# Performance work log

Measured on AMD Instinct MI355X. Metric: run time of the kernel, lower is better.

## Reference

```python
import jax, jax.numpy as jnp
import numpy as np

HEADS = 16
HEAD_DIM = 64
QUAD_C = 5.0   # 2quad: exp(x) ~ (x + c)^2
EPS = 1e-6


def setup_inputs() -> dict:
    key = jax.random.key(0)
    k1, k2, k3 = jax.random.split(key, 3)
    B, T, H = 2, 2048, 1024
    x = jax.random.normal(k1, (B, T, H), dtype=jnp.float32)
    # scaled init to keep pre-activation scores sane
    Wqkv = jax.random.normal(k2, (H, 3 * H), dtype=jnp.float32) * (H ** -0.5)
    Wo = jax.random.normal(k3, (H, H), dtype=jnp.float32) * (H ** -0.5)
    tau = jnp.full((HEADS,), 5.0, dtype=jnp.float32)
    return {"x": x, "Wqkv": Wqkv, "Wo": Wo, "tau": tau}


def reference(x, Wqkv, Wo, tau):
    B, T, C = x.shape
    h, d = HEADS, HEAD_DIM
    qkv = x @ Wqkv                                  # [B,T,3C]
    q, k, v = jnp.split(qkv, 3, axis=-1)
    q = q.reshape(B, T, h, d).transpose(0, 2, 1, 3)  # [B,h,T,d]
    k = k.reshape(B, T, h, d).transpose(0, 2, 1, 3)
    v = v.reshape(B, T, h, d).transpose(0, 2, 1, 3)
    # tau-scaled scores
    s = jnp.einsum("bhqd,bhkd->bhqk", q, k) / (jnp.sqrt(jnp.float32(d)) * tau[None, :, None, None])
    # 2quad attention: (s + c)^2 normalized over keys (non-softmax)
    e = jnp.square(s + QUAD_C)                       # [B,h,T,T], >=0
    w = e / (jnp.sum(e, axis=-1, keepdims=True) + EPS)
    out = jnp.einsum("bhqk,bhkd->bhqd", w, v)        # [B,h,T,d]
    out = out.transpose(0, 2, 1, 3).reshape(B, T, C)
    return out @ Wo
```

## Files before the change

### kernel.cpp

```cpp
#include <hip/hip_runtime.h>
#include <hip/hip_bf16.h>


typedef unsigned short ushort_t;
typedef __attribute__((ext_vector_type(8))) short short8;
typedef __attribute__((ext_vector_type(4))) float f32x4;
typedef __attribute__((ext_vector_type(16))) float f32x16;

#define B_      2
#define T_      2048
#define C_      1024
#define HEADS_  16
#define D_      64

union frag_u { unsigned u[4]; short8 s8; };

__device__ __forceinline__ ushort_t f2bf(float f) {
  __hip_bfloat16 h = __float2bfloat16(f);
  return *reinterpret_cast<ushort_t*>(&h);
}

__device__ __forceinline__ unsigned cvt_pk_bf16(float lo, float hi) {
  unsigned r;
  asm("v_cvt_pk_bf16_f32 %0, %1, %2" : "=v"(r) : "v"(lo), "v"(hi));
  return r;
}

__device__ __forceinline__ void permlane32_swap(unsigned &a, unsigned &b) {
  asm volatile("v_permlane32_swap_b32 %0, %1" : "+v"(a), "+v"(b));
}

__device__ __forceinline__ f32x16 zero16() {
  f32x16 z;
#pragma unroll
  for (int i = 0; i < 16; ++i) z[i] = 0.f;
  return z;
}

__global__ __launch_bounds__(256) void cast_x_kernel(const float* __restrict__ x,
                                                     ushort_t* __restrict__ xb) {
  int i = blockIdx.x * 256 + threadIdx.x;
  float4 f = ((const float4*)x)[i];
  ushort_t* o = xb + (size_t)i * 4;
  o[0] = f2bf(f.x); o[1] = f2bf(f.y); o[2] = f2bf(f.z); o[3] = f2bf(f.w);
}

__global__ __launch_bounds__(256) void transpose_cast_w(const float* __restrict__ in,
                                                        ushort_t* __restrict__ out,
                                                        int R, int Cc) {
  __shared__ float tile[64][65];
  int rb = blockIdx.y, cb = blockIdx.x;
  int c = threadIdx.x & 63;
  int r0 = threadIdx.x >> 6;
#pragma unroll
  for (int i = 0; i < 16; ++i) {
    int r = r0 + i * 4;
    tile[r][c] = in[(size_t)(rb * 64 + r) * Cc + cb * 64 + c];
  }
  __syncthreads();
#pragma unroll
  for (int i = 0; i < 16; ++i) {
    int r = r0 + i * 4;
    out[(size_t)(cb * 64 + r) * R + rb * 64 + c] = f2bf(tile[c][r]);
  }
}

__global__ __launch_bounds__(256) void transpose_v_kernel(const ushort_t* __restrict__ v,
                                                          ushort_t* __restrict__ vT) {
  __shared__ ushort_t tile[64][72];
  int bh = blockIdx.y, tb = blockIdx.x;
  int c = threadIdx.x & 63;
  int r0 = threadIdx.x >> 6;
#pragma unroll
  for (int i = 0; i < 16; ++i) {
    int r = r0 + i * 4;
    tile[r][c] = v[((size_t)bh * T_ + tb * 64 + r) * D_ + c];
  }
  __syncthreads();
#pragma unroll
  for (int i = 0; i < 16; ++i) {
    int r = r0 + i * 4;
    vT[((size_t)bh * D_ + r) * T_ + tb * 64 + c] = tile[c][r];
  }
}

__device__ __forceinline__ void gemm_tile(const ushort_t* __restrict__ A,
                                          const ushort_t* __restrict__ Bt,
                                          int K, int tm, int tn,
                                          ushort_t* lds, f32x4 acc[4][4]) {
  const int tid = threadIdx.x;
  const int lane = tid & 63, wave = tid >> 6;
  const int wm = wave >> 1, wn = wave & 1;
  const int lr = lane & 15, lk = lane >> 4;
  ushort_t* As = lds;
  ushort_t* Bs = lds + 128 * 72;
  const ushort_t* Ag = A + (size_t)tm * 128 * K;
  const ushort_t* Bg = Bt + (size_t)tn * 128 * K;

  for (int kt = 0; kt < K; kt += 64) {
#pragma unroll
    for (int i = 0; i < 4; ++i) {
      int cch = tid + i * 256; int row = cch >> 3, kc = cch & 7;
      *(short8*)&As[row * 72 + kc * 8] =
          *(const short8*)&Ag[(size_t)row * K + kt + kc * 8];
    }
#pragma unroll
    for (int i = 0; i < 4; ++i) {
      int cch = tid + i * 256; int row = cch >> 3, kc = cch & 7;
      *(short8*)&Bs[row * 72 + kc * 8] =
          *(const short8*)&Bg[(size_t)row * K + kt + kc * 8];
    }
    __syncthreads();
#pragma unroll
    for (int kk = 0; kk < 64; kk += 32) {
      short8 a[4], b[4];
#pragma unroll
      for (int m = 0; m < 4; ++m)
        a[m] = *(const short8*)&As[(wm * 64 + m * 16 + lr) * 72 + kk + lk * 8];
#pragma unroll
      for (int n = 0; n < 4; ++n)
        b[n] = *(const short8*)&Bs[(wn * 64 + n * 16 + lr) * 72 + kk + lk * 8];
#pragma unroll
      for (int m = 0; m < 4; ++m)
#pragma unroll
        for (int n = 0; n < 4; ++n)
          acc[m][n] = __builtin_amdgcn_mfma_f32_16x16x32_bf16(a[m], b[n], acc[m][n], 0, 0, 0);
    }
    __syncthreads();
  }
}

__global__ __launch_bounds__(256) void gemm_qkv(const ushort_t* __restrict__ xb,
                                                const ushort_t* __restrict__ wT,
                                                ushort_t* __restrict__ qg,
                                                ushort_t* __restrict__ kg,
                                                ushort_t* __restrict__ vg) {
  __shared__ __align__(16) ushort_t lds[2 * 128 * 72];
  f32x4 acc[4][4];
#pragma unroll
  for (int m = 0; m < 4; ++m)
#pragma unroll
    for (int n = 0; n < 4; ++n) acc[m][n] = (f32x4){0.f, 0.f, 0.f, 0.f};

  gemm_tile(xb, wT, C_, blockIdx.y, blockIdx.x, lds, acc);

  const int lane = threadIdx.x & 63, wave = threadIdx.x >> 6;
  const int wm = wave >> 1, wn = wave & 1;
  const int lr = lane & 15, lk = lane >> 4;
#pragma unroll
  for (int m = 0; m < 4; ++m)
#pragma unroll
    for (int n = 0; n < 4; ++n)
#pragma unroll
      for (int r = 0; r < 4; ++r) {
        int row = blockIdx.y * 128 + wm * 64 + m * 16 + lk * 4 + r;
        int col = blockIdx.x * 128 + wn * 64 + n * 16 + lr;
        int b = row >> 11, t = row & 2047;
        int part = col >> 10, idx = col & 1023;
        int h = idx >> 6, j = idx & 63;
        ushort_t* dst = (part == 0) ? qg : (part == 1) ? kg : vg;
        dst[(((size_t)(b * HEADS_ + h)) * T_ + t) * D_ + j] = f2bf(acc[m][n][r]);
      }
}

__global__ __launch_bounds__(256) void gemm_out(const ushort_t* __restrict__ ab,
                                                const ushort_t* __restrict__ woT,
                                                float* __restrict__ out) {
  __shared__ __align__(16) ushort_t lds[2 * 128 * 72];
  f32x4 acc[4][4];
#pragma unroll
  for (int m = 0; m < 4; ++m)
#pragma unroll
    for (int n = 0; n < 4; ++n) acc[m][n] = (f32x4){0.f, 0.f, 0.f, 0.f};

  gemm_tile(ab, woT, C_, blockIdx.y, blockIdx.x, lds, acc);

  const int lane = threadIdx.x & 63, wave = threadIdx.x >> 6;
  const int wm = wave >> 1, wn = wave & 1;
  const int lr = lane & 15, lk = lane >> 4;
#pragma unroll
  for (int m = 0; m < 4; ++m)
#pragma unroll
    for (int n = 0; n < 4; ++n)
#pragma unroll
      for (int r = 0; r < 4; ++r) {
        int row = blockIdx.y * 128 + wm * 64 + m * 16 + lk * 4 + r;
        int col = blockIdx.x * 128 + wn * 64 + n * 16 + lr;
        out[(size_t)row * C_ + col] = acc[m][n][r];
      }
}

__global__ __launch_bounds__(256, 2) void attn_kernel(const ushort_t* __restrict__ qg,
                                                      const ushort_t* __restrict__ kg,
                                                      const ushort_t* __restrict__ vTg,
                                                      const float* __restrict__ tau,
                                                      ushort_t* __restrict__ attn_out) {
  __shared__ __align__(16) ushort_t kvbuf[128 * 72 + 64 * 136];
  __shared__ float denom_lds[2][2][2][32];
  ushort_t* Ks  = kvbuf;
  ushort_t* Vts = kvbuf + 128 * 72;

  const int tid = threadIdx.x, lane = tid & 63;
  const int w = tid >> 6, wq = w >> 1, wk = w & 1;
  const int l31 = lane & 31, hi = lane >> 5, hi8 = hi * 8;
  const int qt = blockIdx.x, bh = blockIdx.y;
  const int b = bh >> 4, h = bh & 15;
  const float inv = 1.0f / (8.0f * tau[h]);

  const ushort_t* kb_ = kg  + (size_t)bh * T_ * D_;
  const ushort_t* vb_ = vTg + (size_t)bh * D_ * T_;
  const ushort_t* qp  = qg  + ((size_t)bh * T_ + qt * 128 + wq * 64) * D_;

  short8 qf[2][4];
#pragma unroll
  for (int qb = 0; qb < 2; ++qb)
#pragma unroll
    for (int dc = 0; dc < 4; ++dc)
      qf[qb][dc] = *(const short8*)&qp[(qb * 32 + l31) * D_ + dc * 16 + hi8];

  f32x16 acc[2][2];
  acc[0][0] = zero16(); acc[0][1] = zero16();
  acc[1][0] = zero16(); acc[1][1] = zero16();
  float denomp[2] = {0.f, 0.f};

  for (int rnd = 0; rnd < T_ / 128; ++rnd) {
    const int kv0 = rnd * 128;
#pragma unroll
    for (int i = 0; i < 4; ++i) {
      int cch = tid + i * 256;
      int row = cch >> 3, kc = cch & 7;
      *(short8*)&Ks[row * 72 + kc * 8] =
          *(const short8*)&kb_[(size_t)(kv0 + row) * D_ + kc * 8];
    }
#pragma unroll
    for (int i = 0; i < 4; ++i) {
      int cch = tid + i * 256;
      int row = cch >> 4, kc = cch & 15;
      *(short8*)&Vts[row * 136 + kc * 8] =
          *(const short8*)&vb_[(size_t)row * T_ + kv0 + kc * 8];
    }
    __syncthreads();

#pragma unroll
    for (int kb = 0; kb < 2; ++kb) {
      const int krow0 = wk * 64 + kb * 32;
      f32x16 s[2]; s[0] = zero16(); s[1] = zero16();
#pragma unroll
      for (int dc = 0; dc < 4; ++dc) {
        short8 kf = *(const short8*)&Ks[(krow0 + l31) * 72 + dc * 16 + hi8];
        s[0] = __builtin_amdgcn_mfma_f32_32x32x16_bf16(kf, qf[0][dc], s[0], 0, 0, 0);
        s[1] = __builtin_amdgcn_mfma_f32_32x32x16_bf16(kf, qf[1][dc], s[1], 0, 0, 0);
      }

      frag_u ef[2][2];
#pragma unroll
      for (int qb = 0; qb < 2; ++qb) {
        float ev[16];
        float dsum = 0.f;
#pragma unroll
        for (int r = 0; r < 16; ++r) {
          float t = fmaf(s[qb][r], inv, 5.0f);
          ev[r] = t * t;
          dsum += ev[r];
        }
        denomp[qb] += dsum;
        unsigned P[8];
#pragma unroll
        for (int p = 0; p < 8; ++p) P[p] = cvt_pk_bf16(ev[2 * p], ev[2 * p + 1]);
        unsigned a0 = P[0], b0 = P[2]; permlane32_swap(a0, b0);
        unsigned a1 = P[1], b1 = P[3]; permlane32_swap(a1, b1);
        ef[qb][0].u[0] = a0; ef[qb][0].u[1] = a1; ef[qb][0].u[2] = b0; ef[qb][0].u[3] = b1;
        unsigned a2 = P[4], b2 = P[6]; permlane32_swap(a2, b2);
        unsigned a3 = P[5], b3 = P[7]; permlane32_swap(a3, b3);
        ef[qb][1].u[0] = a2; ef[qb][1].u[1] = a3; ef[qb][1].u[2] = b2; ef[qb][1].u[3] = b3;
      }

#pragma unroll
      for (int c = 0; c < 2; ++c)
#pragma unroll
        for (int db = 0; db < 2; ++db) {
          short8 vf = *(const short8*)&Vts[(db * 32 + l31) * 136 + krow0 + c * 16 + hi8];
          acc[0][db] = __builtin_amdgcn_mfma_f32_32x32x16_bf16(ef[0][c].s8, vf, acc[0][db], 0, 0, 0);
          acc[1][db] = __builtin_amdgcn_mfma_f32_32x32x16_bf16(ef[1][c].s8, vf, acc[1][db], 0, 0, 0);
        }
    }
    __syncthreads();
  }

#pragma unroll
  for (int qb = 0; qb < 2; ++qb) {
    float v = denomp[qb];
    v += __shfl_xor(v, 32);
    if (lane < 32) denom_lds[wk][wq][qb][l31] = v;
  }
  float* out_lds = (float*)kvbuf;
  if (wk == 1) {
#pragma unroll
    for (int qb = 0; qb < 2; ++qb)
#pragma unroll
      for (int db = 0; db < 2; ++db)
#pragma unroll
        for (int r = 0; r < 16; ++r) {
          int qr = qb * 32 + (r & 3) + 8 * (r >> 2) + 4 * hi;
          out_lds[(wq * 64 + qr) * 64 + db * 32 + l31] = acc[qb][db][r];
        }
  }
  __syncthreads();
  if (wk == 0) {
#pragma unroll
    for (int qb = 0; qb < 2; ++qb)
#pragma unroll
      for (int r = 0; r < 16; ++r) {
        int cr = (r & 3) + 8 * (r >> 2) + 4 * hi;
        int qr = qb * 32 + cr;
        float dt = denom_lds[0][wq][qb][cr] + denom_lds[1][wq][qb][cr];
        float dinv = 1.0f / (dt + 1e-6f);
#pragma unroll
        for (int db = 0; db < 2; ++db) {
          float val = acc[qb][db][r] + out_lds[(wq * 64 + qr) * 64 + db * 32 + l31];
          int grow = b * T_ + qt * 128 + wq * 64 + qr;
          attn_out[(size_t)grow * C_ + h * 64 + db * 32 + l31] = f2bf(val * dinv);
        }
      }
  }
}

extern "C" void kernel_launch(void* const* d_in, const int* in_sizes, int n_in,
                              void* d_out, int out_size, void* d_ws, size_t ws_size,
                              hipStream_t stream) {
  const float* x    = (const float*)d_in[0];
  const float* Wqkv = (const float*)d_in[1];
  const float* Wo   = (const float*)d_in[2];
  const float* tau  = (const float*)d_in[3];
  float* out = (float*)d_out;

  char* ws = (char*)d_ws;
  ushort_t* xb    = (ushort_t*)(ws);
  ushort_t* wqkvT = (ushort_t*)(ws + 8388608);
  ushort_t* woT   = (ushort_t*)(ws + 14680064);
  ushort_t* qg    = (ushort_t*)(ws + 16777216);
  ushort_t* kg    = (ushort_t*)(ws + 25165824);
  ushort_t* ab    = (ushort_t*)(ws + 33554432);
  ushort_t* vg  = (ushort_t*)d_out;
  ushort_t* vTg = (ushort_t*)d_out + 4194304;

  cast_x_kernel<<<4096, 256, 0, stream>>>(x, xb);
  transpose_cast_w<<<dim3(48, 16), 256, 0, stream>>>(Wqkv, wqkvT, 1024, 3072);
  transpose_cast_w<<<dim3(16, 16), 256, 0, stream>>>(Wo, woT, 1024, 1024);
  gemm_qkv<<<dim3(24, 32), 256, 0, stream>>>(xb, wqkvT, qg, kg, vg);
  transpose_v_kernel<<<dim3(32, 32), 256, 0, stream>>>(vg, vTg);
  attn_kernel<<<dim3(16, 32), 256, 0, stream>>>(qg, kg, vTg, tau, ab);
  gemm_out<<<dim3(8, 32), 256, 0, stream>>>(ab, woT, out);
}
```

Measured before the change: 126.1 us.

## Split attention work across 4 key-slice waves and use direct global-to-LDS loads in GEMMs

The attention kernel now gives each block 64 queries instead of 128, and its four waves each take a 32-key slice of every 128-key tile. The launch grid doubles to 1024 blocks and the occupancy hint rises to 4 blocks per CU. Partial accumulators are combined through a two-stage LDS tree reduction, which adds extra barriers and reloads each K/V tile for half as many queries. Separately, the GEMM tile loader switches to global_load_lds with an unpadded 64-wide LDS layout, skipping the register round trip. That layout may cause LDS bank conflicts on the fragment reads.

```diff
diff --git a/kernel.cpp b/kernel.cpp
--- a/kernel.cpp
+++ b/kernel.cpp
@@ -35,6 +35,12 @@
 #pragma unroll
   for (int i = 0; i < 16; ++i) z[i] = 0.f;
   return z;
+}
+
+__device__ __forceinline__ void gload_lds16(const ushort_t* g, ushort_t* l) {
+  __builtin_amdgcn_global_load_lds(
+      (const __attribute__((address_space(1))) unsigned*)(const void*)g,
+      (__attribute__((address_space(3))) unsigned*)(void*)l, 16, 0, 0);
 }
 
 __global__ __launch_bounds__(256) void cast_x_kernel(const float* __restrict__ x,
@@ -93,22 +99,18 @@
   const int wm = wave >> 1, wn = wave & 1;
   const int lr = lane & 15, lk = lane >> 4;
   ushort_t* As = lds;
-  ushort_t* Bs = lds + 128 * 72;
+  ushort_t* Bs = lds + 128 * 64;
   const ushort_t* Ag = A + (size_t)tm * 128 * K;
   const ushort_t* Bg = Bt + (size_t)tn * 128 * K;
 
   for (int kt = 0; kt < K; kt += 64) {
 #pragma unroll
     for (int i = 0; i < 4; ++i) {
-      int cch = tid + i * 256; int row = cch >> 3, kc = cch & 7;
-      *(short8*)&As[row * 72 + kc * 8] =
-          *(const short8*)&Ag[(size_t)row * K + kt + kc * 8];
-    }
-#pragma unroll
-    for (int i = 0; i < 4; ++i) {
-      int cch = tid + i * 256; int row = cch >> 3, kc = cch & 7;
-      *(short8*)&Bs[row * 72 + kc * 8] =
-          *(const short8*)&Bg[(size_t)row * K + kt + kc * 8];
+      int chunk = wave * 4 + i;
+      int eidx = chunk * 512 + lane * 8;
+      int row = eidx >> 6, col = eidx & 63;
+      gload_lds16(Ag + (size_t)row * K + kt + col, As + eidx);
+      gload_lds16(Bg + (size_t)row * K + kt + col, Bs + eidx);
     }
     __syncthreads();
 #pragma unroll
@@ -116,10 +118,10 @@
       short8 a[4], b[4];
 #pragma unroll
       for (int m = 0; m < 4; ++m)
-        a[m] = *(const short8*)&As[(wm * 64 + m * 16 + lr) * 72 + kk + lk * 8];
+        a[m] = *(const short8*)&As[(wm * 64 + m * 16 + lr) * 64 + kk + lk * 8];
 #pragma unroll
       for (int n = 0; n < 4; ++n)
-        b[n] = *(const short8*)&Bs[(wn * 64 + n * 16 + lr) * 72 + kk + lk * 8];
+        b[n] = *(const short8*)&Bs[(wn * 64 + n * 16 + lr) * 64 + kk + lk * 8];
 #pragma unroll
       for (int m = 0; m < 4; ++m)
 #pragma unroll
@@ -135,7 +137,7 @@
                                                 ushort_t* __restrict__ qg,
                                                 ushort_t* __restrict__ kg,
                                                 ushort_t* __restrict__ vg) {
-  __shared__ __align__(16) ushort_t lds[2 * 128 * 72];
+  __shared__ __align__(16) ushort_t lds[2 * 128 * 64];
   f32x4 acc[4][4];
 #pragma unroll
   for (int m = 0; m < 4; ++m)
@@ -166,7 +168,7 @@
 __global__ __launch_bounds__(256) void gemm_out(const ushort_t* __restrict__ ab,
                                                 const ushort_t* __restrict__ woT,
                                                 float* __restrict__ out) {
-  __shared__ __align__(16) ushort_t lds[2 * 128 * 72];
+  __shared__ __align__(16) ushort_t lds[2 * 128 * 64];
   f32x4 acc[4][4];
 #pragma unroll
   for (int m = 0; m < 4; ++m)
@@ -190,18 +192,18 @@
       }
 }
 
-__global__ __launch_bounds__(256, 2) void attn_kernel(const ushort_t* __restrict__ qg,
+__global__ __launch_bounds__(256, 4) void attn_kernel(const ushort_t* __restrict__ qg,
                                                       const ushort_t* __restrict__ kg,
                                                       const ushort_t* __restrict__ vTg,
                                                       const float* __restrict__ tau,
                                                       ushort_t* __restrict__ attn_out) {
   __shared__ __align__(16) ushort_t kvbuf[128 * 72 + 64 * 136];
-  __shared__ float denom_lds[2][2][2][32];
+  __shared__ float denom_lds[4][2][32];
   ushort_t* Ks  = kvbuf;
   ushort_t* Vts = kvbuf + 128 * 72;
 
   const int tid = threadIdx.x, lane = tid & 63;
-  const int w = tid >> 6, wq = w >> 1, wk = w & 1;
+  const int w = tid >> 6;
   const int l31 = lane & 31, hi = lane >> 5, hi8 = hi * 8;
   const int qt = blockIdx.x, bh = blockIdx.y;
   const int b = bh >> 4, h = bh & 15;
@@ -209,7 +211,7 @@
 
   const ushort_t* kb_ = kg  + (size_t)bh * T_ * D_;
   const ushort_t* vb_ = vTg + (size_t)bh * D_ * T_;
-  const ushort_t* qp  = qg  + ((size_t)bh * T_ + qt * 128 + wq * 64) * D_;
+  const ushort_t* qp  = qg  + ((size_t)bh * T_ + qt * 64) * D_;
 
   short8 qf[2][4];
 #pragma unroll
@@ -222,6 +224,8 @@
   acc[0][0] = zero16(); acc[0][1] = zero16();
   acc[1][0] = zero16(); acc[1][1] = zero16();
   float denomp[2] = {0.f, 0.f};
+
+  const int krow0 = w * 32;
 
   for (int rnd = 0; rnd < T_ / 128; ++rnd) {
     const int kv0 = rnd * 128;
@@ -241,49 +245,45 @@
     }
     __syncthreads();
 
-#pragma unroll
-    for (int kb = 0; kb < 2; ++kb) {
-      const int krow0 = wk * 64 + kb * 32;
-      f32x16 s[2]; s[0] = zero16(); s[1] = zero16();
-#pragma unroll
-      for (int dc = 0; dc < 4; ++dc) {
-        short8 kf = *(const short8*)&Ks[(krow0 + l31) * 72 + dc * 16 + hi8];
-        s[0] = __builtin_amdgcn_mfma_f32_32x32x16_bf16(kf, qf[0][dc], s[0], 0, 0, 0);
-        s[1] = __builtin_amdgcn_mfma_f32_32x32x16_bf16(kf, qf[1][dc], s[1], 0, 0, 0);
-      }
-
-      frag_u ef[2][2];
-#pragma unroll
-      for (int qb = 0; qb < 2; ++qb) {
-        float ev[16];
-        float dsum = 0.f;
-#pragma unroll
-        for (int r = 0; r < 16; ++r) {
-          float t = fmaf(s[qb][r], inv, 5.0f);
-          ev[r] = t * t;
-          dsum += ev[r];
-        }
-        denomp[qb] += dsum;
-        unsigned P[8];
-#pragma unroll
-        for (int p = 0; p < 8; ++p) P[p] = cvt_pk_bf16(ev[2 * p], ev[2 * p + 1]);
-        unsigned a0 = P[0], b0 = P[2]; permlane32_swap(a0, b0);
-        unsigned a1 = P[1], b1 = P[3]; permlane32_swap(a1, b1);
-        ef[qb][0].u[0] = a0; ef[qb][0].u[1] = a1; ef[qb][0].u[2] = b0; ef[qb][0].u[3] = b1;
-        unsigned a2 = P[4], b2 = P[6]; permlane32_swap(a2, b2);
-        unsigned a3 = P[5], b3 = P[7]; permlane32_swap(a3, b3);
-        ef[qb][1].u[0] = a2; ef[qb][1].u[1] = a3; ef[qb][1].u[2] = b2; ef[qb][1].u[3] = b3;
-      }
-
-#pragma unroll
-      for (int c = 0; c < 2; ++c)
-#pragma unroll
-        for (int db = 0; db < 2; ++db) {
-          short8 vf = *(const short8*)&Vts[(db * 32 + l31) * 136 + krow0 + c * 16 + hi8];
-          acc[0][db] = __builtin_amdgcn_mfma_f32_32x32x16_bf16(ef[0][c].s8, vf, acc[0][db], 0, 0, 0);
-          acc[1][db] = __builtin_amdgcn_mfma_f32_32x32x16_bf16(ef[1][c].s8, vf, acc[1][db], 0, 0, 0);
-        }
-    }
+    f32x16 s[2]; s[0] = zero16(); s[1] = zero16();
+#pragma unroll
+    for (int dc = 0; dc < 4; ++dc) {
+      short8 kf = *(const short8*)&Ks[(krow0 + l31) * 72 + dc * 16 + hi8];
+      s[0] = __builtin_amdgcn_mfma_f32_32x32x16_bf16(kf, qf[0][dc], s[0], 0, 0, 0);
+      s[1] = __builtin_amdgcn_mfma_f32_32x32x16_bf16(kf, qf[1][dc], s[1], 0, 0, 0);
+    }
+
+    frag_u ef[2][2];
+#pragma unroll
+    for (int qb = 0; qb < 2; ++qb) {
+      float ev[16];
+      float dsum = 0.f;
+#pragma unroll
+      for (int r = 0; r < 16; ++r) {
+        float t = fmaf(s[qb][r], inv, 5.0f);
+        ev[r] = t * t;
+        dsum += ev[r];
+      }
+      denomp[qb] += dsum;
+      unsigned P[8];
+#pragma unroll
+      for (int p = 0; p < 8; ++p) P[p] = cvt_pk_bf16(ev[2 * p], ev[2 * p + 1]);
+      unsigned a0 = P[0], b0 = P[2]; permlane32_swap(a0, b0);
+      unsigned a1 = P[1], b1 = P[3]; permlane32_swap(a1, b1);
+      ef[qb][0].u[0] = a0; ef[qb][0].u[1] = a1; ef[qb][0].u[2] = b0; ef[qb][0].u[3] = b1;
+      unsigned a2 = P[4], b2 = P[6]; permlane32_swap(a2, b2);
+      unsigned a3 = P[5], b3 = P[7]; permlane32_swap(a3, b3);
+      ef[qb][1].u[0] = a2; ef[qb][1].u[1] = a3; ef[qb][1].u[2] = b2; ef[qb][1].u[3] = b3;
+    }
+
+#pragma unroll
+    for (int c = 0; c < 2; ++c)
+#pragma unroll
+      for (int db = 0; db < 2; ++db) {
+        short8 vf = *(const short8*)&Vts[(db * 32 + l31) * 136 + krow0 + c * 16 + hi8];
+        acc[0][db] = __builtin_amdgcn_mfma_f32_32x32x16_bf16(ef[0][c].s8, vf, acc[0][db], 0, 0, 0);
+        acc[1][db] = __builtin_amdgcn_mfma_f32_32x32x16_bf16(ef[1][c].s8, vf, acc[1][db], 0, 0, 0);
+      }
     __syncthreads();
   }
 
@@ -291,10 +291,10 @@
   for (int qb = 0; qb < 2; ++qb) {
     float v = denomp[qb];
     v += __shfl_xor(v, 32);
-    if (lane < 32) denom_lds[wk][wq][qb][l31] = v;
+    if (lane < 32) denom_lds[w][qb][l31] = v;
   }
   float* out_lds = (float*)kvbuf;
-  if (wk == 1) {
+  if (w >= 2) {
 #pragma unroll
     for (int qb = 0; qb < 2; ++qb)
 #pragma unroll
@@ -302,23 +302,48 @@
 #pragma unroll
         for (int r = 0; r < 16; ++r) {
           int qr = qb * 32 + (r & 3) + 8 * (r >> 2) + 4 * hi;
-          out_lds[(wq * 64 + qr) * 64 + db * 32 + l31] = acc[qb][db][r];
+          out_lds[(w - 2) * 4096 + qr * 64 + db * 32 + l31] = acc[qb][db][r];
         }
   }
   __syncthreads();
-  if (wk == 0) {
+  if (w < 2) {
+#pragma unroll
+    for (int qb = 0; qb < 2; ++qb)
+#pragma unroll
+      for (int db = 0; db < 2; ++db)
+#pragma unroll
+        for (int r = 0; r < 16; ++r) {
+          int qr = qb * 32 + (r & 3) + 8 * (r >> 2) + 4 * hi;
+          acc[qb][db][r] += out_lds[w * 4096 + qr * 64 + db * 32 + l31];
+        }
+  }
+  __syncthreads();
+  if (w == 1) {
+#pragma unroll
+    for (int qb = 0; qb < 2; ++qb)
+#pragma unroll
+      for (int db = 0; db < 2; ++db)
+#pragma unroll
+        for (int r = 0; r < 16; ++r) {
+          int qr = qb * 32 + (r & 3) + 8 * (r >> 2) + 4 * hi;
+          out_lds[qr * 64 + db * 32 + l31] = acc[qb][db][r];
+        }
+  }
+  __syncthreads();
+  if (w == 0) {
 #pragma unroll
     for (int qb = 0; qb < 2; ++qb)
 #pragma unroll
       for (int r = 0; r < 16; ++r) {
         int cr = (r & 3) + 8 * (r >> 2) + 4 * hi;
         int qr = qb * 32 + cr;
-        float dt = denom_lds[0][wq][qb][cr] + denom_lds[1][wq][qb][cr];
+        float dt = denom_lds[0][qb][cr] + denom_lds[1][qb][cr] +
+                   denom_lds[2][qb][cr] + denom_lds[3][qb][cr];
         float dinv = 1.0f / (dt + 1e-6f);
 #pragma unroll
         for (int db = 0; db < 2; ++db) {
-          float val = acc[qb][db][r] + out_lds[(wq * 64 + qr) * 64 + db * 32 + l31];
-          int grow = b * T_ + qt * 128 + wq * 64 + qr;
+          float val = acc[qb][db][r] + out_lds[qr * 64 + db * 32 + l31];
+          int grow = b * T_ + qt * 64 + qr;
           attn_out[(size_t)grow * C_ + h * 64 + db * 32 + l31] = f2bf(val * dinv);
         }
       }
@@ -349,6 +374,6 @@
   transpose_cast_w<<<dim3(16, 16), 256, 0, stream>>>(Wo, woT, 1024, 1024);
   gemm_qkv<<<dim3(24, 32), 256, 0, stream>>>(xb, wqkvT, qg, kg, vg);
   transpose_v_kernel<<<dim3(32, 32), 256, 0, stream>>>(vg, vTg);
-  attn_kernel<<<dim3(16, 32), 256, 0, stream>>>(qg, kg, vTg, tau, ab);
+  attn_kernel<<<dim3(32, 32), 256, 0, stream>>>(qg, kg, vTg, tau, ab);
   gemm_out<<<dim3(8, 32), 256, 0, stream>>>(ab, woT, out);
 }
```

Measured after the change: 284.8 us. 2.26x slower.

## Fuse V transpose into QKV GEMM epilogue and shrink attention blocks

Applied to the files above, without the earlier changes.

The QKV GEMM epilogue now writes V directly in transposed [bh, d, t] layout, so the separate transpose kernel and its extra round trip through memory go away. The attention kernel is restructured to 128-thread blocks, each handling 64 queries with 64-key tiles. That removes the split-K reduction across waves through LDS and doubles the grid size. The trade-offs are that transposed V stores are strided and uncoalesced, and each block reuses K/V less since it serves fewer queries per tile.

```diff
diff --git a/kernel.cpp b/kernel.cpp
--- a/kernel.cpp
+++ b/kernel.cpp
@@ -62,25 +62,6 @@
   for (int i = 0; i < 16; ++i) {
     int r = r0 + i * 4;
     out[(size_t)(cb * 64 + r) * R + rb * 64 + c] = f2bf(tile[c][r]);
-  }
-}
-
-__global__ __launch_bounds__(256) void transpose_v_kernel(const ushort_t* __restrict__ v,
-                                                          ushort_t* __restrict__ vT) {
-  __shared__ ushort_t tile[64][72];
-  int bh = blockIdx.y, tb = blockIdx.x;
-  int c = threadIdx.x & 63;
-  int r0 = threadIdx.x >> 6;
-#pragma unroll
-  for (int i = 0; i < 16; ++i) {
-    int r = r0 + i * 4;
-    tile[r][c] = v[((size_t)bh * T_ + tb * 64 + r) * D_ + c];
-  }
-  __syncthreads();
-#pragma unroll
-  for (int i = 0; i < 16; ++i) {
-    int r = r0 + i * 4;
-    vT[((size_t)bh * D_ + r) * T_ + tb * 64 + c] = tile[c][r];
   }
 }
 
@@ -134,7 +115,7 @@
                                                 const ushort_t* __restrict__ wT,
                                                 ushort_t* __restrict__ qg,
                                                 ushort_t* __restrict__ kg,
-                                                ushort_t* __restrict__ vg) {
+                                                ushort_t* __restrict__ vTg) {
   __shared__ __align__(16) ushort_t lds[2 * 128 * 72];
   f32x4 acc[4][4];
 #pragma unroll
@@ -158,8 +139,11 @@
         int b = row >> 11, t = row & 2047;
         int part = col >> 10, idx = col & 1023;
         int h = idx >> 6, j = idx & 63;
-        ushort_t* dst = (part == 0) ? qg : (part == 1) ? kg : vg;
-        dst[(((size_t)(b * HEADS_ + h)) * T_ + t) * D_ + j] = f2bf(acc[m][n][r]);
+        ushort_t val = f2bf(acc[m][n][r]);
+        size_t bh = (size_t)(b * HEADS_ + h);
+        if (part == 0)      qg[(bh * T_ + t) * D_ + j] = val;
+        else if (part == 1) kg[(bh * T_ + t) * D_ + j] = val;
+        else                vTg[(bh * D_ + j) * T_ + t] = val;
       }
 }
 
@@ -190,18 +174,17 @@
       }
 }
 
-__global__ __launch_bounds__(256, 2) void attn_kernel(const ushort_t* __restrict__ qg,
+__global__ __launch_bounds__(128, 2) void attn_kernel(const ushort_t* __restrict__ qg,
                                                       const ushort_t* __restrict__ kg,
                                                       const ushort_t* __restrict__ vTg,
                                                       const float* __restrict__ tau,
                                                       ushort_t* __restrict__ attn_out) {
-  __shared__ __align__(16) ushort_t kvbuf[128 * 72 + 64 * 136];
-  __shared__ float denom_lds[2][2][2][32];
-  ushort_t* Ks  = kvbuf;
-  ushort_t* Vts = kvbuf + 128 * 72;
+  __shared__ __align__(16) ushort_t Ks[64 * 72];
+  __shared__ __align__(16) ushort_t Vts[64 * 72];
+  __shared__ float denom_sh[2][32];
 
   const int tid = threadIdx.x, lane = tid & 63;
-  const int w = tid >> 6, wq = w >> 1, wk = w & 1;
+  const int w = tid >> 6;
   const int l31 = lane & 31, hi = lane >> 5, hi8 = hi * 8;
   const int qt = blockIdx.x, bh = blockIdx.y;
   const int b = bh >> 4, h = bh & 15;
@@ -209,120 +192,88 @@
 
   const ushort_t* kb_ = kg  + (size_t)bh * T_ * D_;
   const ushort_t* vb_ = vTg + (size_t)bh * D_ * T_;
-  const ushort_t* qp  = qg  + ((size_t)bh * T_ + qt * 128 + wq * 64) * D_;
-
-  short8 qf[2][4];
-#pragma unroll
-  for (int qb = 0; qb < 2; ++qb)
-#pragma unroll
-    for (int dc = 0; dc < 4; ++dc)
-      qf[qb][dc] = *(const short8*)&qp[(qb * 32 + l31) * D_ + dc * 16 + hi8];
-
-  f32x16 acc[2][2];
-  acc[0][0] = zero16(); acc[0][1] = zero16();
-  acc[1][0] = zero16(); acc[1][1] = zero16();
-  float denomp[2] = {0.f, 0.f};
-
-  for (int rnd = 0; rnd < T_ / 128; ++rnd) {
-    const int kv0 = rnd * 128;
-#pragma unroll
-    for (int i = 0; i < 4; ++i) {
-      int cch = tid + i * 256;
-      int row = cch >> 3, kc = cch & 7;
-      *(short8*)&Ks[row * 72 + kc * 8] =
-          *(const short8*)&kb_[(size_t)(kv0 + row) * D_ + kc * 8];
-    }
-#pragma unroll
-    for (int i = 0; i < 4; ++i) {
-      int cch = tid + i * 256;
-      int row = cch >> 4, kc = cch & 15;
-      *(short8*)&Vts[row * 136 + kc * 8] =
-          *(const short8*)&vb_[(size_t)row * T_ + kv0 + kc * 8];
+  const ushort_t* qp  = qg  + ((size_t)bh * T_ + qt * 64 + w * 32) * D_;
+
+  short8 qf[4];
+#pragma unroll
+  for (int dc = 0; dc < 4; ++dc)
+    qf[dc] = *(const short8*)&qp[l31 * D_ + dc * 16 + hi8];
+
+  f32x16 acc[2];
+  acc[0] = zero16(); acc[1] = zero16();
+  float denomp = 0.f;
+
+  for (int kv0 = 0; kv0 < T_; kv0 += 64) {
+#pragma unroll
+    for (int p = 0; p < 4; ++p) {
+      int idx = p * 1024 + tid * 8;
+      int row = idx >> 6, col = idx & 63;
+      *(short8*)&Ks[row * 72 + col] =
+          *(const short8*)&kb_[(size_t)(kv0 + row) * D_ + col];
+    }
+#pragma unroll
+    for (int p = 0; p < 4; ++p) {
+      int idx = p * 1024 + tid * 8;
+      int row = idx >> 6, col = idx & 63;
+      *(short8*)&Vts[row * 72 + col] =
+          *(const short8*)&vb_[(size_t)row * T_ + kv0 + col];
     }
     __syncthreads();
 
 #pragma unroll
     for (int kb = 0; kb < 2; ++kb) {
-      const int krow0 = wk * 64 + kb * 32;
-      f32x16 s[2]; s[0] = zero16(); s[1] = zero16();
+      f32x16 s = zero16();
 #pragma unroll
       for (int dc = 0; dc < 4; ++dc) {
-        short8 kf = *(const short8*)&Ks[(krow0 + l31) * 72 + dc * 16 + hi8];
-        s[0] = __builtin_amdgcn_mfma_f32_32x32x16_bf16(kf, qf[0][dc], s[0], 0, 0, 0);
-        s[1] = __builtin_amdgcn_mfma_f32_32x32x16_bf16(kf, qf[1][dc], s[1], 0, 0, 0);
+        short8 kf = *(const short8*)&Ks[(kb * 32 + l31) * 72 + dc * 16 + hi8];
+        s = __builtin_amdgcn_mfma_f32_32x32x16_bf16(kf, qf[dc], s, 0, 0, 0);
       }
 
-      frag_u ef[2][2];
-#pragma unroll
-      for (int qb = 0; qb < 2; ++qb) {
-        float ev[16];
-        float dsum = 0.f;
-#pragma unroll
-        for (int r = 0; r < 16; ++r) {
-          float t = fmaf(s[qb][r], inv, 5.0f);
-          ev[r] = t * t;
-          dsum += ev[r];
-        }
-        denomp[qb] += dsum;
-        unsigned P[8];
-#pragma unroll
-        for (int p = 0; p < 8; ++p) P[p] = cvt_pk_bf16(ev[2 * p], ev[2 * p + 1]);
-        unsigned a0 = P[0], b0 = P[2]; permlane32_swap(a0, b0);
-        unsigned a1 = P[1], b1 = P[3]; permlane32_swap(a1, b1);
-        ef[qb][0].u[0] = a0; ef[qb][0].u[1] = a1; ef[qb][0].u[2] = b0; ef[qb][0].u[3] = b1;
-        unsigned a2 = P[4], b2 = P[6]; permlane32_swap(a2, b2);
-        unsigned a3 = P[5], b3 = P[7]; permlane32_swap(a3, b3);
-        ef[qb][1].u[0] = a2; ef[qb][1].u[1] = a3; ef[qb][1].u[2] = b2; ef[qb][1].u[3] = b3;
+      float ev[16];
+      float dsum = 0.f;
+#pragma unroll
+      for (int r = 0; r < 16; ++r) {
+        float t = fmaf(s[r], inv, 5.0f);
+        ev[r] = t * t;
+        dsum += ev[r];
       }
+      denomp += dsum;
+      unsigned P[8];
+#pragma unroll
+      for (int p = 0; p < 8; ++p) P[p] = cvt_pk_bf16(ev[2 * p], ev[2 * p + 1]);
+      frag_u ef[2];
+      unsigned a0 = P[0], b0 = P[2]; permlane32_swap(a0, b0);
+      unsigned a1 = P[1], b1 = P[3]; permlane32_swap(a1, b1);
+      ef[0].u[0] = a0; ef[0].u[1] = a1; ef[0].u[2] = b0; ef[0].u[3] = b1;
+      unsigned a2 = P[4], b2 = P[6]; permlane32_swap(a2, b2);
+      unsigned a3 = P[5], b3 = P[7]; permlane32_swap(a3, b3);
+      ef[1].u[0] = a2; ef[1].u[1] = a3; ef[1].u[2] = b2; ef[1].u[3] = b3;
 
 #pragma unroll
       for (int c = 0; c < 2; ++c)
 #pragma unroll
         for (int db = 0; db < 2; ++db) {
-          short8 vf = *(const short8*)&Vts[(db * 32 + l31) * 136 + krow0 + c * 16 + hi8];
-          acc[0][db] = __builtin_amdgcn_mfma_f32_32x32x16_bf16(ef[0][c].s8, vf, acc[0][db], 0, 0, 0);
-          acc[1][db] = __builtin_amdgcn_mfma_f32_32x32x16_bf16(ef[1][c].s8, vf, acc[1][db], 0, 0, 0);
+          short8 vf = *(const short8*)&Vts[(db * 32 + l31) * 72 + kb * 32 + c * 16 + hi8];
+          acc[db] = __builtin_amdgcn_mfma_f32_32x32x16_bf16(ef[c].s8, vf, acc[db], 0, 0, 0);
         }
     }
     __syncthreads();
   }
 
-#pragma unroll
-  for (int qb = 0; qb < 2; ++qb) {
-    float v = denomp[qb];
-    v += __shfl_xor(v, 32);
-    if (lane < 32) denom_lds[wk][wq][qb][l31] = v;
-  }
-  float* out_lds = (float*)kvbuf;
-  if (wk == 1) {
-#pragma unroll
-    for (int qb = 0; qb < 2; ++qb)
-#pragma unroll
-      for (int db = 0; db < 2; ++db)
-#pragma unroll
-        for (int r = 0; r < 16; ++r) {
-          int qr = qb * 32 + (r & 3) + 8 * (r >> 2) + 4 * hi;
-          out_lds[(wq * 64 + qr) * 64 + db * 32 + l31] = acc[qb][db][r];
-        }
-  }
+  float dv = denomp + __shfl_xor(denomp, 32);
+  if (lane < 32) denom_sh[w][l31] = dv;
   __syncthreads();
-  if (wk == 0) {
-#pragma unroll
-    for (int qb = 0; qb < 2; ++qb)
-#pragma unroll
-      for (int r = 0; r < 16; ++r) {
-        int cr = (r & 3) + 8 * (r >> 2) + 4 * hi;
-        int qr = qb * 32 + cr;
-        float dt = denom_lds[0][wq][qb][cr] + denom_lds[1][wq][qb][cr];
-        float dinv = 1.0f / (dt + 1e-6f);
-#pragma unroll
-        for (int db = 0; db < 2; ++db) {
-          float val = acc[qb][db][r] + out_lds[(wq * 64 + qr) * 64 + db * 32 + l31];
-          int grow = b * T_ + qt * 128 + wq * 64 + qr;
-          attn_out[(size_t)grow * C_ + h * 64 + db * 32 + l31] = f2bf(val * dinv);
-        }
-      }
-  }
+
+#pragma unroll
+  for (int db = 0; db < 2; ++db)
+#pragma unroll
+    for (int r = 0; r < 16; ++r) {
+      int qlocal = (r & 3) + 8 * (r >> 2) + 4 * hi;
+      float dt = denom_sh[w][qlocal];
+      float o = acc[db][r] / (dt + 1e-6f);
+      int grow = b * T_ + qt * 64 + w * 32 + qlocal;
+      attn_out[(size_t)grow * C_ + h * 64 + db * 32 + l31] = f2bf(o);
+    }
 }
 
 extern "C" void kernel_launch(void* const* d_in, const int* in_sizes, int n_in,
@@ -341,14 +292,12 @@
   ushort_t* qg    = (ushort_t*)(ws + 16777216);
   ushort_t* kg    = (ushort_t*)(ws + 25165824);
   ushort_t* ab    = (ushort_t*)(ws + 33554432);
-  ushort_t* vg  = (ushort_t*)d_out;
-  ushort_t* vTg = (ushort_t*)d_out + 4194304;
+  ushort_t* vTg = (ushort_t*)d_out;
 
   cast_x_kernel<<<4096, 256, 0, stream>>>(x, xb);
   transpose_cast_w<<<dim3(48, 16), 256, 0, stream>>>(Wqkv, wqkvT, 1024, 3072);
   transpose_cast_w<<<dim3(16, 16), 256, 0, stream>>>(Wo, woT, 1024, 1024);
-  gemm_qkv<<<dim3(24, 32), 256, 0, stream>>>(xb, wqkvT, qg, kg, vg);
-  transpose_v_kernel<<<dim3(32, 32), 256, 0, stream>>>(vg, vTg);
-  attn_kernel<<<dim3(16, 32), 256, 0, stream>>>(qg, kg, vTg, tau, ab);
+  gemm_qkv<<<dim3(24, 32), 256, 0, stream>>>(xb, wqkvT, qg, kg, vTg);
+  attn_kernel<<<dim3(32, 32), 128, 0, stream>>>(qg, kg, vTg, tau, ab);
   gemm_out<<<dim3(8, 32), 256, 0, stream>>>(ab, woT, out);
 }
```

Result: slower. 204.2 us (+61.9%).

## Load K/V MFMA fragments directly from global memory, dropping LDS staging

Applied to the files above, without the earlier changes.

Removes the cooperative LDS staging of K and V^T tiles and the two per-round block barriers. Each wave now reads its K and V fragments straight from global memory (through L1/L2) into registers for the MFMA operands. This cuts LDS traffic and synchronisation, but each K/V element is now fetched from global by both q-waves, and the V^T reads are strided rows. Latency hiding then depends on occupancy and cache hit rates.

```diff
diff --git a/kernel.cpp b/kernel.cpp
--- a/kernel.cpp
+++ b/kernel.cpp
@@ -195,10 +195,8 @@
                                                       const ushort_t* __restrict__ vTg,
                                                       const float* __restrict__ tau,
                                                       ushort_t* __restrict__ attn_out) {
-  __shared__ __align__(16) ushort_t kvbuf[128 * 72 + 64 * 136];
+  __shared__ float out_lds[2 * 64 * 64];
   __shared__ float denom_lds[2][2][2][32];
-  ushort_t* Ks  = kvbuf;
-  ushort_t* Vts = kvbuf + 128 * 72;
 
   const int tid = threadIdx.x, lane = tid & 63;
   const int w = tid >> 6, wq = w >> 1, wk = w & 1;
@@ -218,6 +216,9 @@
     for (int dc = 0; dc < 4; ++dc)
       qf[qb][dc] = *(const short8*)&qp[(qb * 32 + l31) * D_ + dc * 16 + hi8];
 
+  const ushort_t* kfp = kb_ + (size_t)(wk * 64 + l31) * D_ + hi8;
+  const ushort_t* vfp = vb_ + (size_t)l31 * T_ + wk * 64 + hi8;
+
   f32x16 acc[2][2];
   acc[0][0] = zero16(); acc[0][1] = zero16();
   acc[1][0] = zero16(); acc[1][1] = zero16();
@@ -226,28 +227,14 @@
   for (int rnd = 0; rnd < T_ / 128; ++rnd) {
     const int kv0 = rnd * 128;
 #pragma unroll
-    for (int i = 0; i < 4; ++i) {
-      int cch = tid + i * 256;
-      int row = cch >> 3, kc = cch & 7;
-      *(short8*)&Ks[row * 72 + kc * 8] =
-          *(const short8*)&kb_[(size_t)(kv0 + row) * D_ + kc * 8];
-    }
-#pragma unroll
-    for (int i = 0; i < 4; ++i) {
-      int cch = tid + i * 256;
-      int row = cch >> 4, kc = cch & 15;
-      *(short8*)&Vts[row * 136 + kc * 8] =
-          *(const short8*)&vb_[(size_t)row * T_ + kv0 + kc * 8];
-    }
-    __syncthreads();
-
-#pragma unroll
     for (int kb = 0; kb < 2; ++kb) {
-      const int krow0 = wk * 64 + kb * 32;
+      const size_t koff = (size_t)(kv0 + kb * 32) * D_;
+      const size_t voff = (size_t)(kv0 + kb * 32);
+
       f32x16 s[2]; s[0] = zero16(); s[1] = zero16();
 #pragma unroll
       for (int dc = 0; dc < 4; ++dc) {
-        short8 kf = *(const short8*)&Ks[(krow0 + l31) * 72 + dc * 16 + hi8];
+        short8 kf = *(const short8*)&kfp[koff + dc * 16];
         s[0] = __builtin_amdgcn_mfma_f32_32x32x16_bf16(kf, qf[0][dc], s[0], 0, 0, 0);
         s[1] = __builtin_amdgcn_mfma_f32_32x32x16_bf16(kf, qf[1][dc], s[1], 0, 0, 0);
       }
@@ -279,12 +266,11 @@
       for (int c = 0; c < 2; ++c)
 #pragma unroll
         for (int db = 0; db < 2; ++db) {
-          short8 vf = *(const short8*)&Vts[(db * 32 + l31) * 136 + krow0 + c * 16 + hi8];
+          short8 vf = *(const short8*)&vfp[(size_t)(db * 32) * T_ + voff + c * 16];
           acc[0][db] = __builtin_amdgcn_mfma_f32_32x32x16_bf16(ef[0][c].s8, vf, acc[0][db], 0, 0, 0);
           acc[1][db] = __builtin_amdgcn_mfma_f32_32x32x16_bf16(ef[1][c].s8, vf, acc[1][db], 0, 0, 0);
         }
     }
-    __syncthreads();
   }
 
 #pragma unroll
@@ -293,7 +279,6 @@
     v += __shfl_xor(v, 32);
     if (lane < 32) denom_lds[wk][wq][qb][l31] = v;
   }
-  float* out_lds = (float*)kvbuf;
   if (wk == 1) {
 #pragma unroll
     for (int qb = 0; qb < 2; ++qb)
```

Result: slower. 155.3 us (+23.1%).
